# Optimization experiments

Measured on AMD Instinct MI355X. Metric: run time of the kernel, lower is better.

Reference implementation:

```python
import jax, jax.numpy as jnp
import numpy as np

HEAD_CHOICES = [8, 10, 12]
MAX_HEADS = 12
HEAD_DIM = 64
MAX_REL_POS = 14
SCALE = HEAD_DIM ** -0.5


def _rel_indices(N):
    # AutoFormer RelativePosition2D_super index computation (static, numpy).
    L = N - 1                      # remove cls token
    s = int(L ** 0.5)              # patches per row
    r = np.arange(L)
    dv = r[None, :] // s - r[:, None] // s
    dh = r[None, :] % s - r[:, None] % s
    iv = np.clip(dv, -MAX_REL_POS, MAX_REL_POS) + MAX_REL_POS + 1
    ih = np.clip(dh, -MAX_REL_POS, MAX_REL_POS) + MAX_REL_POS + 1
    iv = np.pad(iv, ((1, 0), (1, 0)))  # cls token row/col -> index 0
    ih = np.pad(ih, ((1, 0), (1, 0)))
    return jnp.asarray(iv), jnp.asarray(ih)


def setup_inputs() -> dict:
    key = jax.random.key(0)
    ks = jax.random.split(key, 6)
    B, N = 16, 577
    T = 2 * MAX_REL_POS + 2  # 30
    x = jax.random.normal(ks[0], (B, N, 3 * MAX_HEADS * HEAD_DIM), dtype=jnp.float32)
    weights = jax.nn.softmax(jax.random.normal(ks[1], (len(HEAD_CHOICES),), dtype=jnp.float32))
    rel_k_table_v = jax.random.normal(ks[2], (T, HEAD_DIM), dtype=jnp.float32) * 0.02
    rel_k_table_h = jax.random.normal(ks[3], (T, HEAD_DIM), dtype=jnp.float32) * 0.02
    rel_v_table_v = jax.random.normal(ks[4], (T, HEAD_DIM), dtype=jnp.float32) * 0.02
    rel_v_table_h = jax.random.normal(ks[5], (T, HEAD_DIM), dtype=jnp.float32) * 0.02
    return dict(x=x, weights=weights,
                rel_k_table_v=rel_k_table_v, rel_k_table_h=rel_k_table_h,
                rel_v_table_v=rel_v_table_v, rel_v_table_h=rel_v_table_h)


def reference(x, weights, rel_k_table_v, rel_k_table_h, rel_v_table_v, rel_v_table_h):
    B, N, _ = x.shape
    # [3, B, H, N, D]
    qkv = x.reshape(B, N, 3, MAX_HEADS, HEAD_DIM).transpose(2, 0, 3, 1, 4)
    # Mixture over head-count choices: slicing first c heads, scaling by w[i],
    # padding to max_heads, and summing == per-head weight sum_i w[i]*[h < c_i].
    head_mask = jnp.asarray(np.array([[1.0 if h < c else 0.0 for h in range(MAX_HEADS)]
                                      for c in HEAD_CHOICES]), dtype=x.dtype)  # [C, H]
    w_head = weights @ head_mask  # [H]
    w4 = w_head[None, :, None, None]
    q = qkv[0] * w4
    k = qkv[1] * w4
    v = qkv[2] * w4
    # content attention + relative-position K bias
    attn = jnp.einsum('bhnd,bhmd->bhnm', q, k) * SCALE
    iv, ih = _rel_indices(N)
    rel_k = rel_k_table_v[iv] + rel_k_table_h[ih]  # [N, N, D]
    attn = attn + jnp.einsum('bhnd,nmd->bhnm', q, rel_k) * SCALE
    attn = jax.nn.softmax(attn, axis=-1)  # attn_drop has p=0 (eval)
    out = jnp.einsum('bhnm,bhmd->bhnd', attn, v)
    rel_v = rel_v_table_v[iv] + rel_v_table_h[ih]  # [N, N, D]
    out = out + jnp.einsum('bhnm,nmd->bhnd', attn, rel_v)
    return out.transpose(0, 2, 1, 3).reshape(B, N, MAX_HEADS * HEAD_DIM)
```

## Files before the change

### kernel.cpp

```cpp
#include <hip/hip_runtime.h>

typedef short bf16x8_t __attribute__((ext_vector_type(8)));
typedef float f32x4_t __attribute__((ext_vector_type(4)));

#define NTOK 577
#define QPAD 640
#define MPAD 608
#define NSTEP 19
#define VTILES 80
#define VTILE_ELEMS 6144

__device__ __forceinline__ unsigned short f2bf(float f) {
  unsigned u = __builtin_bit_cast(unsigned, f);
  u += 0x7FFFu + ((u >> 16) & 1u);
  return (unsigned short)(u >> 16);
}
__device__ __forceinline__ float headw(const float* wts, int h) {
  float w0 = wts[0], w1 = wts[1], w2 = wts[2];
  return (h < 8) ? (w0 + w1 + w2) : ((h < 10) ? (w1 + w2) : w2);
}
__device__ __forceinline__ unsigned rangemask(int lo, int hi) {
  lo = lo < 0 ? 0 : lo; hi = hi > 32 ? 32 : hi;
  if (hi <= lo) return 0u;
  unsigned mh = (hi >= 32) ? 0xFFFFFFFFu : ((1u << hi) - 1u);
  unsigned ml = (1u << lo) - 1u;
  return mh & ~ml;
}

extern "C" __global__ __launch_bounds__(256) void prep_x3(
    const float* __restrict__ x, const float* __restrict__ wts,
    unsigned short* __restrict__ qbf, unsigned short* __restrict__ kbf,
    unsigned short* __restrict__ vbf) {
  __shared__ unsigned short vT[8][768];
  const int tid = threadIdx.x;
  const int mc = blockIdx.x;
  const int n0 = mc * 8;
  const int b = blockIdx.y;
  const float w0 = wts[0], w1 = wts[1], w2 = wts[2];
  const float wA = w0 + w1 + w2, wB = w1 + w2, wC = w2;
  const float* xb = x + (size_t)b * NTOK * 2304;
#pragma unroll 2
  for (int p = 0; p < 18; ++p) {
    int i = p * 256 + tid;
    int nl = i / 576;
    int c4 = i - nl * 576;
    int n = n0 + nl;
    float4 v = {0.f, 0.f, 0.f, 0.f};
    if (n < NTOK) v = *(const float4*)(xb + (size_t)n * 2304 + c4 * 4);
    int sec = c4 / 192;
    int cc = c4 - sec * 192;
    int h = cc >> 4, d4 = cc & 15;
    if (sec == 2) {
      ushort4 o;
      o.x = f2bf(v.x); o.y = f2bf(v.y); o.z = f2bf(v.z); o.w = f2bf(v.w);
      *(ushort4*)&vT[nl][cc * 4] = o;
    } else {
      float s = 1.f;
      if (sec == 0) {
        float w = (h < 8) ? wA : ((h < 10) ? wB : wC);
        s = w * w * 0.125f;
      }
      ushort4 o;
      o.x = f2bf(v.x * s); o.y = f2bf(v.y * s); o.z = f2bf(v.z * s); o.w = f2bf(v.w * s);
      unsigned short* dst = (sec == 0) ? qbf : kbf;
      *(ushort4*)(dst + ((size_t)(b * 12 + h)) * QPAD * 64 + (size_t)n * 64 + d4 * 4) = o;
    }
  }
  __syncthreads();
  unsigned short* tile = vbf + (size_t)(b * VTILES + mc) * VTILE_ELEMS;
#pragma unroll
  for (int t = 0; t < 3; ++t) {
    int hd = t * 256 + tid;
    bf16x8_t val;
#pragma unroll
    for (int jj = 0; jj < 8; ++jj) val[jj] = (short)vT[jj][hd];
    *(bf16x8_t*)(tile + (size_t)hd * 8) = val;
  }
}

extern "C" __global__ __launch_bounds__(256) void prep_tab(
    const float* __restrict__ wts,
    const float* __restrict__ tkv, const float* __restrict__ tkh,
    const float* __restrict__ tvv, const float* __restrict__ tvh,
    unsigned short* __restrict__ tkb, unsigned short* __restrict__ tvb,
    unsigned short* __restrict__ gfb) {
  int tid = threadIdx.x, bx = blockIdx.x;
  if (bx < 48) {
    int cid = bx * 256 + tid;
    int d4 = cid & 15, t = (cid >> 4) & 31, tb = (cid >> 9) & 1, h = cid >> 10;
    float s = 1.f / headw(wts, h);
    const float* src = tb ? tkh : tkv;
    float4 v = {0,0,0,0};
    if (t < 30) v = *(const float4*)(src + t * 64 + d4 * 4);
    ushort4 o;
    o.x = f2bf(v.x * s); o.y = f2bf(v.y * s); o.z = f2bf(v.z * s); o.w = f2bf(v.w * s);
    *(ushort4*)(tkb + (((size_t)(h * 2 + tb)) * 32 + t) * 64 + d4 * 4) = o;
  } else if (bx == 48) {
    for (int i = 0; i < 16; ++i) {
      int id = tid * 16 + i;
      int t = id & 31, d = (id >> 5) & 63, tb = id >> 11;
      const float* src = tb ? tvh : tvv;
      tvb[id] = (t < 30) ? f2bf(src[t * 64 + d]) : (unsigned short)0;
    }
  } else {
    int id = (bx - 49) * 256 + tid;
    int lane = id & 63, gt = (id >> 6) & 1;
    int sg = id >> 7;
    int step = sg % 19, tb = sg / 19;
    int l15 = lane & 15, quad = lane >> 4;
    int g = gt * 16 + l15;
    int m0 = step * 32;
    unsigned mask = 0u;
    if (g < 25) {
      if (g == 24) {
        mask = rangemask(NTOK - m0, MPAD - m0);
        if (step == 0) mask |= 1u;
      } else if (tb == 0) {
        mask = rangemask(24 * g + 1 - m0, 24 * g + 25 - m0);
      } else {
        int j0 = (g + 1 - m0) % 24; if (j0 < 0) j0 += 24;
        for (int j = j0; j < 32; j += 24) {
          int m = m0 + j;
          if (m >= 1 && m < NTOK) mask |= (1u << j);
        }
      }
    }
    unsigned short o[8];
#pragma unroll
    for (int j = 0; j < 8; ++j) {
      int m_loc = quad * 8 + j;
      o[j] = ((mask >> m_loc) & 1u) ? (unsigned short)0x3F80 : (unsigned short)0;
    }
    *(ushort4*)(gfb + (size_t)id * 8) = *(ushort4*)&o[0];
    *(ushort4*)(gfb + (size_t)id * 8 + 4) = *(ushort4*)&o[4];
  }
}

struct __align__(16) SMem {
  float qg_s[2][64][25];
  float l_s[64];
  union {
    struct { float qv_t[2][64][30]; } pro;
    struct {
      unsigned short k_s[32][76];
      unsigned short v_sT[64][44];
      unsigned short P_s[64][44];
    } loop;
    struct { float sv_f[2][64][30]; } epi;
  } u;
};

extern "C" __global__ __launch_bounds__(256, 5) void hma_kernel(
    const unsigned short* __restrict__ qbf, const unsigned short* __restrict__ kbf,
    const unsigned short* __restrict__ vbf, const unsigned short* __restrict__ tkb,
    const unsigned short* __restrict__ tvb, const unsigned short* __restrict__ gfb,
    const float* __restrict__ wts, float* __restrict__ out) {
  __shared__ SMem sm;
  const int tid = threadIdx.x;
  const int wave = tid >> 6, lane = tid & 63, quad = lane >> 4, l15 = lane & 15;
  const int rg = wave & 1;
  const int cg = wave >> 1;
  const int tb_w = cg;
  const int n0 = blockIdx.x * 64;
  const int h = blockIdx.y, b = blockIdx.z;
  const float w = headw(wts, h);

  const unsigned short* qb = qbf + ((size_t)(b * 12 + h)) * QPAD * 64;
  const unsigned short* kb = kbf + ((size_t)(b * 12 + h)) * QPAD * 64;
  const unsigned short* vb = vbf + (size_t)b * VTILES * VTILE_ELEMS + (size_t)h * 512;
  const unsigned short* gfp = gfb + ((size_t)tb_w * 19) * 1024 + lane * 8;

  bf16x8_t qa[2][2];
  for (int sub = 0; sub < 2; ++sub)
    for (int kk = 0; kk < 2; ++kk)
      qa[sub][kk] = *(const bf16x8_t*)(qb + (size_t)(n0 + rg * 32 + sub * 16 + l15) * 64 + kk * 32 + quad * 8);

  {
    const unsigned short* tkp = tkb + ((size_t)(h * 2 + tb_w)) * 32 * 64;
    for (int tt = 0; tt < 2; ++tt) {
      for (int sub = 0; sub < 2; ++sub) {
        f32x4_t acc = {0.f, 0.f, 0.f, 0.f};
        for (int kk = 0; kk < 2; ++kk) {
          bf16x8_t bb = *(const bf16x8_t*)(tkp + (size_t)(tt * 16 + l15) * 64 + kk * 32 + quad * 8);
          acc = __builtin_amdgcn_mfma_f32_16x16x32_bf16(qa[sub][kk], bb, acc, 0, 0, 0);
        }
        int t = tt * 16 + l15;
        if (t < 30)
          for (int r = 0; r < 4; ++r)
            sm.u.pro.qv_t[tb_w][rg * 32 + sub * 16 + quad * 4 + r][t] = acc[r];
      }
    }
  }
  __syncthreads();
  for (int p = tid; p < 2 * 64 * 25; p += 256) {
    int tb = p / 1600, r2 = p % 1600, n = r2 / 25, g = r2 % 25;
    int n_g = n0 + n;
    int t;
    if (n_g == 0 || n_g >= NTOK || g == 24) t = 0;
    else {
      int base = tb ? ((n_g - 1) % 24) : ((n_g - 1) / 24);
      int dq = g - base; dq = dq < -14 ? -14 : (dq > 14 ? 14 : dq);
      t = dq + 15;
    }
    sm.qg_s[tb][n][g] = sm.u.pro.qv_t[tb][n][t];
  }

  const int m_loc = cg * 16 + l15;
  int rmv, cmv;
  if (m_loc == 0) { rmv = 0; cmv = -1; }
  else { rmv = (m_loc - 1) / 24; cmv = (m_loc - 1) - rmv * 24; }
  const bool cls_lane = (m_loc == 0);

  f32x4_t oacc[2][2] = {{{0,0,0,0},{0,0,0,0}},{{0,0,0,0},{0,0,0,0}}};
  f32x4_t rsacc[2][2] = {{{0,0,0,0},{0,0,0,0}},{{0,0,0,0},{0,0,0,0}}};

  const int krow = tid >> 3, kch = tid & 7;
  const int vrow = tid >> 2, vch = tid & 3;
  const unsigned short* kptr = kb + (size_t)krow * 64 + kch * 8;
  const unsigned short* vptr = vb + (size_t)vch * VTILE_ELEMS + vrow * 8;
  bf16x8_t kreg = *(const bf16x8_t*)kptr;
  bf16x8_t vreg = *(const bf16x8_t*)vptr;

  for (int step = 0; step < NSTEP; ++step) {
    const int m0 = step * 32;
    __syncthreads();
    *(bf16x8_t*)&sm.u.loop.k_s[krow][kch * 8] = kreg;
    *(bf16x8_t*)&sm.u.loop.v_sT[vrow][vch * 8] = vreg;
    __syncthreads();
    kreg = *(const bf16x8_t*)(kptr + (size_t)(m0 + 32) * 64);
    vreg = *(const bf16x8_t*)(vptr + (size_t)(m0 + 32) * 768);
    bf16x8_t gv0 = *(const bf16x8_t*)(gfp + (size_t)step * 1024);
    bf16x8_t gv1 = *(const bf16x8_t*)(gfp + (size_t)step * 1024 + 512);
    f32x4_t s[2] = {{0,0,0,0},{0,0,0,0}};
    {
      bf16x8_t kb0 = *(const bf16x8_t*)&sm.u.loop.k_s[cg * 16 + l15][quad * 8];
      bf16x8_t kb1 = *(const bf16x8_t*)&sm.u.loop.k_s[cg * 16 + l15][32 + quad * 8];
      for (int sub = 0; sub < 2; ++sub) {
        s[sub] = __builtin_amdgcn_mfma_f32_16x16x32_bf16(qa[sub][0], kb0, s[sub], 0, 0, 0);
        s[sub] = __builtin_amdgcn_mfma_f32_16x16x32_bf16(qa[sub][1], kb1, s[sub], 0, 0, 0);
      }
    }
    const int m_g = m0 + m_loc;
    int ur = rmv, uc = cmv;
    if (cls_lane && step == 0) { ur = 24; uc = 24; }
    const bool mpad = (m_g >= NTOK);
    for (int sub = 0; sub < 2; ++sub)
      for (int r = 0; r < 4; ++r) {
        int n_loc = rg * 32 + sub * 16 + quad * 4 + r;
        float logit = s[sub][r] + sm.qg_s[0][n_loc][ur] + sm.qg_s[1][n_loc][uc];
        float p = __expf(logit);
        if (mpad) p = 0.f;
        unsigned u = __builtin_bit_cast(unsigned, p);
        sm.u.loop.P_s[n_loc][m_loc] = (unsigned short)((u + 0x8000u) >> 16);
      }
    { int c = cmv + 8; int carry = (c >= 24); cmv = carry ? c - 24 : c; rmv += 1 + carry; }
    __syncthreads();
    bf16x8_t pa[2];
    for (int sub = 0; sub < 2; ++sub)
      pa[sub] = *(const bf16x8_t*)&sm.u.loop.P_s[rg * 32 + sub * 16 + l15][quad * 8];
    for (int ds = 0; ds < 2; ++ds) {
      bf16x8_t bb = *(const bf16x8_t*)&sm.u.loop.v_sT[cg * 32 + ds * 16 + l15][quad * 8];
      for (int sub = 0; sub < 2; ++sub)
        oacc[sub][ds] = __builtin_amdgcn_mfma_f32_16x16x32_bf16(pa[sub], bb, oacc[sub][ds], 0, 0, 0);
    }
    for (int sub = 0; sub < 2; ++sub) {
      rsacc[sub][0] = __builtin_amdgcn_mfma_f32_16x16x32_bf16(pa[sub], gv0, rsacc[sub][0], 0, 0, 0);
      rsacc[sub][1] = __builtin_amdgcn_mfma_f32_16x16x32_bf16(pa[sub], gv1, rsacc[sub][1], 0, 0, 0);
    }
  }

  __syncthreads();
  for (int e = tid; e < 2 * 64 * 30; e += 256) (&sm.u.epi.sv_f[0][0][0])[e] = 0.f;
  __syncthreads();
  for (int sub = 0; sub < 2; ++sub)
    for (int gt = 0; gt < 2; ++gt) {
      int g = gt * 16 + l15;
      if (g < 25) {
        for (int r = 0; r < 4; ++r) {
          int n_loc = rg * 32 + sub * 16 + quad * 4 + r;
          int n_g = n0 + n_loc;
          int t;
          if (n_g == 0 || n_g >= NTOK || g == 24) t = 0;
          else {
            int base = tb_w ? ((n_g - 1) % 24) : ((n_g - 1) / 24);
            int dq = g - base; dq = dq < -14 ? -14 : (dq > 14 ? 14 : dq);
            t = dq + 15;
          }
          atomicAdd(&sm.u.epi.sv_f[tb_w][n_loc][t], rsacc[sub][gt][r]);
        }
      }
    }
  __syncthreads();
  if (tid < 64) {
    float l = 0.f;
    for (int t = 0; t < 30; ++t) l += sm.u.epi.sv_f[0][tid][t];
    sm.l_s[tid] = l;
  }
  for (int sub = 0; sub < 2; ++sub)
    for (int ds = 0; ds < 2; ++ds)
      for (int r = 0; r < 4; ++r) oacc[sub][ds][r] *= w;
  for (int tb = 0; tb < 2; ++tb) {
    bf16x8_t av[2];
    for (int sub = 0; sub < 2; ++sub) {
      int n_loc = rg * 32 + sub * 16 + l15;
      for (int j = 0; j < 8; ++j) {
        int t = quad * 8 + j;
        float f = (t < 30) ? sm.u.epi.sv_f[tb][n_loc][t] : 0.f;
        unsigned u = __builtin_bit_cast(unsigned, f);
        av[sub][j] = (short)((u + 0x8000u) >> 16);
      }
    }
    for (int ds = 0; ds < 2; ++ds) {
      bf16x8_t bb = *(const bf16x8_t*)(tvb + ((size_t)(tb * 64 + cg * 32 + ds * 16 + l15)) * 32 + quad * 8);
      for (int sub = 0; sub < 2; ++sub)
        oacc[sub][ds] = __builtin_amdgcn_mfma_f32_16x16x32_bf16(av[sub], bb, oacc[sub][ds], 0, 0, 0);
    }
  }
  __syncthreads();
  float* ob = out + (size_t)b * NTOK * 768 + h * 64;
  for (int sub = 0; sub < 2; ++sub)
    for (int r = 0; r < 4; ++r) {
      int n_loc = rg * 32 + sub * 16 + quad * 4 + r;
      int n_g = n0 + n_loc;
      if (n_g < NTOK) {
        float inv = 1.f / sm.l_s[n_loc];
        for (int ds = 0; ds < 2; ++ds) {
          int d = cg * 32 + ds * 16 + l15;
          ob[(size_t)n_g * 768 + d] = oacc[sub][ds][r] * inv;
        }
      }
    }
}

extern "C" void kernel_launch(void* const* d_in, const int* in_sizes, int n_in,
                              void* d_out, int out_size, void* d_ws, size_t ws_size,
                              hipStream_t stream) {
  const float* x   = (const float*)d_in[0];
  const float* wts = (const float*)d_in[1];
  const float* tkv = (const float*)d_in[2];
  const float* tkh = (const float*)d_in[3];
  const float* tvv = (const float*)d_in[4];
  const float* tvh = (const float*)d_in[5];
  float* out = (float*)d_out;
  const int B = in_sizes[0] / (NTOK * 2304);

  unsigned short* ws = (unsigned short*)d_ws;
  size_t qkSz = (size_t)B * 12 * QPAD * 64;
  unsigned short* qbf = ws;
  unsigned short* kbf = ws + qkSz;
  unsigned short* vbf = ws + 2 * qkSz;
  unsigned short* tkb = vbf + qkSz;
  unsigned short* tvb = tkb + (size_t)12 * 2 * 32 * 64;
  unsigned short* gfb = tvb + (size_t)2 * 64 * 32;

  prep_x3<<<dim3(VTILES, B), 256, 0, stream>>>(x, wts, qbf, kbf, vbf);
  prep_tab<<<dim3(68, 1, 1), 256, 0, stream>>>(wts, tkv, tkh, tvv, tvh, tkb, tvb, gfb);
  hma_kernel<<<dim3(10, 12, B), 256, 0, stream>>>(qbf, kbf, vbf, tkb, tvb, gfb, wts, out);
}
```

Baseline: 255.7 us.

## Load K/V MFMA fragments directly from global, double-buffer P, remap workgroups

K and V operands are now read straight from global memory into MFMA fragment registers instead of being staged through LDS. That removes the shared-memory copies and one of the two barriers per step, and double-buffering P_s keeps the single remaining barrier safe. The relative-position gather table is transposed so each lane reads a float4 instead of four scalar LDS loads. Workgroup IDs are remapped with an XCD-style interleave for cache locality, and launch bounds drop to 4 waves per SIMD. The trade-off is higher register pressure and more uncoalesced global loads in exchange for fewer barriers and less LDS traffic.

Measured after the change: 251.4 us. About the same (-1.6%).

```diff
diff --git a/kernel.cpp b/kernel.cpp
--- a/kernel.cpp
+++ b/kernel.cpp
@@ -137,20 +137,16 @@
 }
 
 struct __align__(16) SMem {
-  float qg_s[2][64][25];
+  float qg_t[2][25][68];
   float l_s[64];
   union {
     struct { float qv_t[2][64][30]; } pro;
-    struct {
-      unsigned short k_s[32][76];
-      unsigned short v_sT[64][44];
-      unsigned short P_s[64][44];
-    } loop;
+    struct { unsigned short P_s[2][64][44]; } loop;
     struct { float sv_f[2][64][30]; } epi;
   } u;
 };
 
-extern "C" __global__ __launch_bounds__(256, 5) void hma_kernel(
+extern "C" __global__ __launch_bounds__(256, 4) void hma_kernel(
     const unsigned short* __restrict__ qbf, const unsigned short* __restrict__ kbf,
     const unsigned short* __restrict__ vbf, const unsigned short* __restrict__ tkb,
     const unsigned short* __restrict__ tvb, const unsigned short* __restrict__ gfb,
@@ -161,13 +157,16 @@
   const int rg = wave & 1;
   const int cg = wave >> 1;
   const int tb_w = cg;
-  const int n0 = blockIdx.x * 64;
-  const int h = blockIdx.y, b = blockIdx.z;
+  const int nwg = gridDim.x * gridDim.y * gridDim.z;
+  const int L = blockIdx.x + gridDim.x * (blockIdx.y + gridDim.y * blockIdx.z);
+  const int wid = (L & 7) * (nwg >> 3) + (L >> 3);
+  const int n0 = (wid % 10) * 64;
+  const int rest = wid / 10;
+  const int h = rest % 12, b = rest / 12;
   const float w = headw(wts, h);
 
   const unsigned short* qb = qbf + ((size_t)(b * 12 + h)) * QPAD * 64;
   const unsigned short* kb = kbf + ((size_t)(b * 12 + h)) * QPAD * 64;
-  const unsigned short* vb = vbf + (size_t)b * VTILES * VTILE_ELEMS + (size_t)h * 512;
   const unsigned short* gfp = gfb + ((size_t)tb_w * 19) * 1024 + lane * 8;
 
   bf16x8_t qa[2][2];
@@ -192,8 +191,8 @@
     }
   }
   __syncthreads();
-  for (int p = tid; p < 2 * 64 * 25; p += 256) {
-    int tb = p / 1600, r2 = p % 1600, n = r2 / 25, g = r2 % 25;
+  for (int p = tid; p < 2 * 25 * 64; p += 256) {
+    int tb = p / 1600, r2 = p % 1600, g = r2 / 64, n = r2 % 64;
     int n_g = n0 + n;
     int t;
     if (n_g == 0 || n_g >= NTOK || g == 24) t = 0;
@@ -202,8 +201,9 @@
       int dq = g - base; dq = dq < -14 ? -14 : (dq > 14 ? 14 : dq);
       t = dq + 15;
     }
-    sm.qg_s[tb][n][g] = sm.u.pro.qv_t[tb][n][t];
-  }
+    sm.qg_t[tb][g][n] = sm.u.pro.qv_t[tb][n][t];
+  }
+  __syncthreads();
 
   const int m_loc = cg * 16 + l15;
   int rmv, cmv;
@@ -214,54 +214,51 @@
   f32x4_t oacc[2][2] = {{{0,0,0,0},{0,0,0,0}},{{0,0,0,0},{0,0,0,0}}};
   f32x4_t rsacc[2][2] = {{{0,0,0,0},{0,0,0,0}},{{0,0,0,0},{0,0,0,0}}};
 
-  const int krow = tid >> 3, kch = tid & 7;
-  const int vrow = tid >> 2, vch = tid & 3;
-  const unsigned short* kptr = kb + (size_t)krow * 64 + kch * 8;
-  const unsigned short* vptr = vb + (size_t)vch * VTILE_ELEMS + vrow * 8;
-  bf16x8_t kreg = *(const bf16x8_t*)kptr;
-  bf16x8_t vreg = *(const bf16x8_t*)vptr;
+  const unsigned short* kfr = kb + (size_t)(cg * 16 + l15) * 64 + quad * 8;
+  const unsigned short* vfr = vbf + (size_t)b * VTILES * VTILE_ELEMS + h * 512
+                              + (size_t)(cg * 32 + l15) * 8;
+  bf16x8_t kf0 = *(const bf16x8_t*)(kfr);
+  bf16x8_t kf1 = *(const bf16x8_t*)(kfr + 32);
 
   for (int step = 0; step < NSTEP; ++step) {
     const int m0 = step * 32;
-    __syncthreads();
-    *(bf16x8_t*)&sm.u.loop.k_s[krow][kch * 8] = kreg;
-    *(bf16x8_t*)&sm.u.loop.v_sT[vrow][vch * 8] = vreg;
-    __syncthreads();
-    kreg = *(const bf16x8_t*)(kptr + (size_t)(m0 + 32) * 64);
-    vreg = *(const bf16x8_t*)(vptr + (size_t)(m0 + 32) * 768);
+    const int buf = step & 1;
     bf16x8_t gv0 = *(const bf16x8_t*)(gfp + (size_t)step * 1024);
     bf16x8_t gv1 = *(const bf16x8_t*)(gfp + (size_t)step * 1024 + 512);
     f32x4_t s[2] = {{0,0,0,0},{0,0,0,0}};
-    {
-      bf16x8_t kb0 = *(const bf16x8_t*)&sm.u.loop.k_s[cg * 16 + l15][quad * 8];
-      bf16x8_t kb1 = *(const bf16x8_t*)&sm.u.loop.k_s[cg * 16 + l15][32 + quad * 8];
-      for (int sub = 0; sub < 2; ++sub) {
-        s[sub] = __builtin_amdgcn_mfma_f32_16x16x32_bf16(qa[sub][0], kb0, s[sub], 0, 0, 0);
-        s[sub] = __builtin_amdgcn_mfma_f32_16x16x32_bf16(qa[sub][1], kb1, s[sub], 0, 0, 0);
-      }
-    }
+    for (int sub = 0; sub < 2; ++sub) {
+      s[sub] = __builtin_amdgcn_mfma_f32_16x16x32_bf16(qa[sub][0], kf0, s[sub], 0, 0, 0);
+      s[sub] = __builtin_amdgcn_mfma_f32_16x16x32_bf16(qa[sub][1], kf1, s[sub], 0, 0, 0);
+    }
+    const unsigned short* vt = vfr + (size_t)(m0 / 8 + quad) * VTILE_ELEMS;
+    bf16x8_t vf0 = *(const bf16x8_t*)(vt);
+    bf16x8_t vf1 = *(const bf16x8_t*)(vt + 128);
+    kf0 = *(const bf16x8_t*)(kfr + (size_t)(m0 + 32) * 64);
+    kf1 = *(const bf16x8_t*)(kfr + (size_t)(m0 + 32) * 64 + 32);
     const int m_g = m0 + m_loc;
     int ur = rmv, uc = cmv;
     if (cls_lane && step == 0) { ur = 24; uc = 24; }
     const bool mpad = (m_g >= NTOK);
-    for (int sub = 0; sub < 2; ++sub)
+    for (int sub = 0; sub < 2; ++sub) {
+      int nbase = rg * 32 + sub * 16 + quad * 4;
+      f32x4_t g0 = *(const f32x4_t*)&sm.qg_t[0][ur][nbase];
+      f32x4_t g1 = *(const f32x4_t*)&sm.qg_t[1][uc][nbase];
       for (int r = 0; r < 4; ++r) {
-        int n_loc = rg * 32 + sub * 16 + quad * 4 + r;
-        float logit = s[sub][r] + sm.qg_s[0][n_loc][ur] + sm.qg_s[1][n_loc][uc];
+        float logit = s[sub][r] + g0[r] + g1[r];
         float p = __expf(logit);
         if (mpad) p = 0.f;
         unsigned u = __builtin_bit_cast(unsigned, p);
-        sm.u.loop.P_s[n_loc][m_loc] = (unsigned short)((u + 0x8000u) >> 16);
-      }
+        sm.u.loop.P_s[buf][nbase + r][m_loc] = (unsigned short)((u + 0x8000u) >> 16);
+      }
+    }
     { int c = cmv + 8; int carry = (c >= 24); cmv = carry ? c - 24 : c; rmv += 1 + carry; }
     __syncthreads();
     bf16x8_t pa[2];
     for (int sub = 0; sub < 2; ++sub)
-      pa[sub] = *(const bf16x8_t*)&sm.u.loop.P_s[rg * 32 + sub * 16 + l15][quad * 8];
-    for (int ds = 0; ds < 2; ++ds) {
-      bf16x8_t bb = *(const bf16x8_t*)&sm.u.loop.v_sT[cg * 32 + ds * 16 + l15][quad * 8];
-      for (int sub = 0; sub < 2; ++sub)
-        oacc[sub][ds] = __builtin_amdgcn_mfma_f32_16x16x32_bf16(pa[sub], bb, oacc[sub][ds], 0, 0, 0);
+      pa[sub] = *(const bf16x8_t*)&sm.u.loop.P_s[buf][rg * 32 + sub * 16 + l15][quad * 8];
+    for (int sub = 0; sub < 2; ++sub) {
+      oacc[sub][0] = __builtin_amdgcn_mfma_f32_16x16x32_bf16(pa[sub], vf0, oacc[sub][0], 0, 0, 0);
+      oacc[sub][1] = __builtin_amdgcn_mfma_f32_16x16x32_bf16(pa[sub], vf1, oacc[sub][1], 0, 0, 0);
     }
     for (int sub = 0; sub < 2; ++sub) {
       rsacc[sub][0] = __builtin_amdgcn_mfma_f32_16x16x32_bf16(pa[sub], gv0, rsacc[sub][0], 0, 0, 0);
```
